# Performance work log

Hardware: AMD Instinct MI355X
Metric: run time of the kernel (lower is better)

The kernel has to match this reference:

```python
import jax, jax.numpy as jnp
import numpy as np

D = 2048      # d_model
H = 16        # kv_heads
G = 4         # num_groups
HPG = H // G  # heads per group
HD = D // H   # head dim = 128
B, S = 2, 2048


def setup_inputs() -> dict:
    key = jax.random.key(0)
    ks = jax.random.split(key, 5)
    def w(k, shape, fan_in):
        return jax.random.normal(k, shape, jnp.float32) * (fan_in ** -0.5)
    return {
        "x": jax.random.normal(ks[0], (B, S, D), jnp.float32),
        "attn_mask": jnp.ones((S, S), jnp.float32),
        "Wqkv": w(ks[1], (D, 3 * D), D),
        "bqkv": jnp.zeros((3 * D,), jnp.float32),
        "Wq": w(ks[2], (G, HD, HD), HD),   # shared per-group query proj
        "bq": jnp.zeros((G, HD), jnp.float32),
        "Wv": w(ks[3], (G, HD, HD), HD),   # shared per-group value proj
        "bv": jnp.zeros((G, HD), jnp.float32),
    }


def reference(x, attn_mask, Wqkv, bqkv, Wq, bq, Wv, bv):
    Bx, Sx, Dm = x.shape
    qkv = x @ Wqkv + bqkv                      # [B,S,3D]
    q, k, v = jnp.split(qkv, 3, axis=-1)       # each [B,S,D]
    q = q.reshape(Bx, Sx, G, HPG, HD)
    k = k.reshape(Bx, Sx, G, HPG, HD)
    v = v.reshape(Bx, Sx, G, HPG, HD)
    # shared per-group linear applied to every head slice in the group
    q = jnp.einsum('bsghd,gde->bsghe', q, Wq) + bq[None, None, :, None, :]
    v = jnp.einsum('bsghd,gde->bsghe', v, Wv) + bv[None, None, :, None, :]
    scale = HD ** -0.5
    scores = jnp.einsum('bqghd,bkghd->bghqk', q, k) * scale   # [B,G,HPG,S,S]
    attn = jax.nn.softmax(scores, axis=-1)
    attn = attn * attn_mask                    # post-softmax multiplicative mask
    out = jnp.einsum('bghqk,bkghd->bqghd', attn, v)            # [B,S,G,HPG,HD]
    return out.reshape(Bx, Sx, Dm)
```

## Files before the change

### kernel.cpp

```cpp
#include <hip/hip_runtime.h>

typedef __attribute__((ext_vector_type(8))) short short8;
typedef __attribute__((ext_vector_type(4))) float f32x4;
typedef __attribute__((ext_vector_type(4))) unsigned short ushort4v;
typedef unsigned long long u64;

#define DM 2048
#define ND 6144
#define SEQ 2048
#define HD 128
#define QSCALE (0.08838834764831845f * 1.4426950408889634f)

#define MFMA(a, b, c) __builtin_amdgcn_mfma_f32_16x16x32_bf16((a), (b), (c), 0, 0, 0)

__device__ __forceinline__ unsigned short f2bf(float f) {
  unsigned int u = __float_as_uint(f);
  return (unsigned short)((u + 0x7FFFu + ((u >> 16) & 1u)) >> 16);
}
__device__ __forceinline__ float bf2f(unsigned short h) {
  return __uint_as_float(((unsigned int)h) << 16);
}

__global__ void cvt_bf16_kernel(const float* __restrict__ src,
                                unsigned short* __restrict__ dst, int n4) {
  int i = blockIdx.x * blockDim.x + threadIdx.x;
  int st = gridDim.x * blockDim.x;
  for (; i < n4; i += st) {
    f32x4 v = ((const f32x4*)src)[i];
    ushort4v o;
    o[0] = f2bf(v[0]); o[1] = f2bf(v[1]); o[2] = f2bf(v[2]); o[3] = f2bf(v[3]);
    ((ushort4v*)dst)[i] = o;
  }
}

__global__ void transk_kernel(const float* __restrict__ Wqkv,
                              unsigned short* __restrict__ WbT) {
  __shared__ float tile[64 * 68];
  int bx = blockIdx.x;
  int dt = bx >> 5, ct = bx & 31;
  int d0 = dt * 64, c0 = ct * 64;
  int t = threadIdx.x;
#pragma unroll
  for (int j = 0; j < 4; ++j) {
    int el = (t + j * 256) * 4;
    int r = el >> 6, cc = el & 63;
    f32x4 v = *(const f32x4*)(Wqkv + (size_t)(d0 + r) * ND + 2048 + c0 + cc);
    *(f32x4*)(&tile[r * 68 + cc]) = v;
  }
  __syncthreads();
#pragma unroll
  for (int j = 0; j < 4; ++j) {
    int el = (t + j * 256) * 4;
    int c = el >> 6, dd = el & 63;
    ushort4v o;
#pragma unroll
    for (int i = 0; i < 4; ++i) o[i] = f2bf(tile[(dd + i) * 68 + c]);
    *(ushort4v*)(&WbT[(size_t)(2048 + c0 + c) * DM + d0 + dd]) = o;
  }
}

__global__ __launch_bounds__(256) void fold_kernel(const float* __restrict__ Wqkv,
                                                   const float* __restrict__ Wq,
                                                   const float* __restrict__ Wv,
                                                   unsigned short* __restrict__ WbT) {
  __shared__ float wm[128 * 64];
  __shared__ float wt[64 * 128];
  int bx = blockIdx.x;
  int p = bx >> 10;
  int head = (bx >> 6) & 15;
  int dt = (bx >> 1) & 31;
  int eh = bx & 1;
  int g = head >> 2;
  const float* Wm = (p ? Wv : Wq) + g * 16384;
  int cbase = p * 4096 + head * 128;
  int d0 = dt * 64;
  int t = threadIdx.x;
#pragma unroll
  for (int j = 0; j < 8; ++j) {
    int el = (t + j * 256) * 4;
    int dd = el >> 6, e = el & 63;
    *(f32x4*)(&wm[dd * 64 + e]) = *(const f32x4*)(Wm + dd * 128 + eh * 64 + e);
  }
#pragma unroll
  for (int j = 0; j < 8; ++j) {
    int el = (t + j * 256) * 4;
    int r = el >> 7, cc = el & 127;
    *(f32x4*)(&wt[r * 128 + cc]) =
        *(const f32x4*)(Wqkv + (size_t)(d0 + r) * ND + cbase + cc);
  }
  __syncthreads();
  int td = t >> 4, te = t & 15;
  int dl = td * 4, e0 = te * 4;
  float acc[4][4];
#pragma unroll
  for (int i = 0; i < 4; ++i)
#pragma unroll
    for (int j = 0; j < 4; ++j) acc[i][j] = 0.f;
  for (int dd = 0; dd < 128; ++dd) {
    f32x4 bv = *(const f32x4*)(&wm[dd * 64 + e0]);
#pragma unroll
    for (int i = 0; i < 4; ++i) {
      float a = wt[(dl + i) * 128 + dd];
#pragma unroll
      for (int j = 0; j < 4; ++j) acc[i][j] += a * bv[j];
    }
  }
  float sc = p ? 1.0f : QSCALE;
  int outcol0 = p * 4096 + head * 128 + eh * 64 + e0;
#pragma unroll
  for (int j = 0; j < 4; ++j) {
    ushort4v o;
#pragma unroll
    for (int i = 0; i < 4; ++i) o[i] = f2bf(acc[i][j] * sc);
    *(ushort4v*)(&WbT[(size_t)(outcol0 + j) * DM + d0 + dl]) = o;
  }
}

__global__ void bias_kernel(const float* __restrict__ bqkv, const float* __restrict__ Wq,
                            const float* __restrict__ bq, const float* __restrict__ Wv,
                            const float* __restrict__ bv, float* __restrict__ biasf) {
  int col = blockIdx.x * 256 + threadIdx.x;
  if (col >= ND) return;
  float v;
  if (col < 2048) {
    int g = col >> 9, e = col & 127, base = col & ~127;
    float s = 0.f;
    for (int dd = 0; dd < 128; ++dd) s += bqkv[base + dd] * Wq[g * 16384 + dd * 128 + e];
    v = (s + bq[g * 128 + e]) * QSCALE;
  } else if (col < 4096) {
    v = bqkv[col];
  } else {
    int cv = col - 4096;
    int g = cv >> 9, e = cv & 127, base = col & ~127;
    float s = 0.f;
    for (int dd = 0; dd < 128; ++dd) s += bqkv[base + dd] * Wv[g * 16384 + dd * 128 + e];
    v = s + bv[g * 128 + e];
  }
  biasf[col] = v;
}

__global__ __launch_bounds__(256) void gemm_kernel(
    const unsigned short* __restrict__ A, const unsigned short* __restrict__ Bt,
    const float* __restrict__ biasf, unsigned short* __restrict__ Qb,
    unsigned short* __restrict__ Kb, unsigned short* __restrict__ Vt) {
  __shared__ unsigned short As[128 * 32];
  __shared__ unsigned short Bs[128 * 32];
  int bid = blockIdx.x;
  int swz = (bid & 7) * 192 + (bid >> 3);
  int bm = swz & 31, bn = swz >> 5;
  int m0 = bm * 128, n0 = bn * 128;
  int tid = threadIdx.x, w = tid >> 6, l = tid & 63;
  int ln = l & 15, hi = l >> 4;
  int wr = w >> 1, wc = w & 1;

  int ob0 = w * 2048 + l * 16;
  int ob1 = ob0 + 1024;
  const unsigned short* a0 = A + (size_t)(m0 + (ob0 >> 6)) * DM + ((ob0 & 63) >> 1);
  const unsigned short* a1 = A + (size_t)(m0 + (ob1 >> 6)) * DM + ((ob1 & 63) >> 1);
  const unsigned short* b0 = Bt + (size_t)(n0 + (ob0 >> 6)) * DM + ((ob0 & 63) >> 1);
  const unsigned short* b1 = Bt + (size_t)(n0 + (ob1 >> 6)) * DM + ((ob1 & 63) >> 1);
  char* asb = (char*)(&As[0]);
  char* bsb = (char*)(&Bs[0]);

  f32x4 acc[4][4] = {};
  for (int kt = 0; kt < DM; kt += 32) {
    __syncthreads();
    __builtin_amdgcn_global_load_lds((const __attribute__((address_space(1))) void*)(a0 + kt),
                                     (__attribute__((address_space(3))) void*)(asb + w * 2048), 16, 0, 0);
    __builtin_amdgcn_global_load_lds((const __attribute__((address_space(1))) void*)(a1 + kt),
                                     (__attribute__((address_space(3))) void*)(asb + w * 2048 + 1024), 16, 0, 0);
    __builtin_amdgcn_global_load_lds((const __attribute__((address_space(1))) void*)(b0 + kt),
                                     (__attribute__((address_space(3))) void*)(bsb + w * 2048), 16, 0, 0);
    __builtin_amdgcn_global_load_lds((const __attribute__((address_space(1))) void*)(b1 + kt),
                                     (__attribute__((address_space(3))) void*)(bsb + w * 2048 + 1024), 16, 0, 0);
    __syncthreads();
    short8 af[4], bfm[4];
#pragma unroll
    for (int mi = 0; mi < 4; ++mi)
      af[mi] = *(const short8*)(&As[(wr * 64 + mi * 16 + ln) * 32 + hi * 8]);
#pragma unroll
    for (int ni = 0; ni < 4; ++ni)
      bfm[ni] = *(const short8*)(&Bs[(wc * 64 + ni * 16 + ln) * 32 + hi * 8]);
#pragma unroll
    for (int mi = 0; mi < 4; ++mi)
#pragma unroll
      for (int ni = 0; ni < 4; ++ni)
        acc[mi][ni] = MFMA(af[mi], bfm[ni], acc[mi][ni]);
  }

  int part = bn >> 4, head = bn & 15;
  int hbuf = (m0 >> 11) * 16 + head;
  int srow0 = (m0 & 2047) + wr * 64;
#pragma unroll
  for (int ni = 0; ni < 4; ++ni) {
    int col = wc * 64 + ni * 16 + ln;
    float bsv = biasf[n0 + col];
#pragma unroll
    for (int mi = 0; mi < 4; ++mi) {
      int srow = srow0 + mi * 16 + hi * 4;
      f32x4 v = acc[mi][ni];
      if (part == 2) {
        ushort4v o = {f2bf(v[0] + bsv), f2bf(v[1] + bsv), f2bf(v[2] + bsv), f2bf(v[3] + bsv)};
        *(ushort4v*)(&Vt[(size_t)(hbuf * 128 + col) * SEQ + srow]) = o;
      } else {
        unsigned short* dst = (part ? Kb : Qb) + ((size_t)hbuf * SEQ + srow) * HD + col;
        dst[0] = f2bf(v[0] + bsv);
        dst[HD] = f2bf(v[1] + bsv);
        dst[2 * HD] = f2bf(v[2] + bsv);
        dst[3 * HD] = f2bf(v[3] + bsv);
      }
    }
  }
}

__global__ __launch_bounds__(256, 2) void attn_kernel(
    const unsigned short* __restrict__ Qb, const unsigned short* __restrict__ Kb,
    const unsigned short* __restrict__ Vt, const unsigned short* __restrict__ Mb,
    float* __restrict__ out) {
  __shared__ unsigned short Ks[64 * 128];
  __shared__ unsigned short Vs[128 * 64];
  __shared__ unsigned short Ms[128 * 64];
  __shared__ unsigned short Ps[4][32 * 64];
  int bx = blockIdx.x;
  int hb = bx >> 4;
  int q0 = (bx & 15) * 128;
  int b = hb >> 4, head = hb & 15;
  int tid = threadIdx.x, w = tid >> 6, l = tid & 63;
  int ln = l & 15, hi = l >> 4;
  const unsigned short* Qh = Qb + ((size_t)hb * SEQ + q0 + w * 32) * HD;
  const unsigned short* Kh = Kb + (size_t)hb * SEQ * HD;
  const unsigned short* Vh = Vt + (size_t)hb * HD * SEQ;
  char* KsB = (char*)(&Ks[0]);
  char* VsB = (char*)(&Vs[0]);
  char* MsB = (char*)(&Ms[0]);
  char* PwB = (char*)(&Ps[w][0]);

  short8 qf[2][4];
#pragma unroll
  for (int qb = 0; qb < 2; ++qb)
#pragma unroll
    for (int kk = 0; kk < 4; ++kk)
      qf[qb][kk] = *(const short8*)(Qh + (qb * 16 + ln) * HD + kk * 32 + hi * 8);

  f32x4 acc[8][2] = {};
  float mrun[2] = {-1e30f, -1e30f}, Zrun[2] = {0.f, 0.f};

  for (int t = 0; t < 32; ++t) {
    int k0 = t * 64;
    __syncthreads();
    {
      int row = tid >> 2, seg = (tid & 3) * 64;
      const unsigned short* src = Kh + (size_t)(k0 + row) * HD + (seg >> 1);
      short8 tv[4];
#pragma unroll
      for (int j = 0; j < 4; ++j) tv[j] = *(const short8*)(src + j * 8);
#pragma unroll
      for (int j = 0; j < 4; ++j)
        *(short8*)(KsB + ((row * 256 + seg + j * 16) ^ ((row & 7) << 4))) = tv[j];
    }
    {
      int row = tid >> 1, seg = (tid & 1) * 64;
      const unsigned short* src = Vh + (size_t)row * SEQ + k0 + (seg >> 1);
      short8 tv[4];
#pragma unroll
      for (int j = 0; j < 4; ++j) tv[j] = *(const short8*)(src + j * 8);
#pragma unroll
      for (int j = 0; j < 4; ++j)
        *(short8*)(VsB + ((row * 128 + seg + j * 16) ^ ((row & 7) << 4))) = tv[j];
    }
    {
      int row = tid >> 1, seg = (tid & 1) * 64;
      const unsigned short* src = Mb + (size_t)(q0 + row) * SEQ + k0 + (seg >> 1);
      short8 tv[4];
#pragma unroll
      for (int j = 0; j < 4; ++j) tv[j] = *(const short8*)(src + j * 8);
#pragma unroll
      for (int j = 0; j < 4; ++j)
        *(short8*)(MsB + ((row * 128 + seg + j * 16) ^ ((row & 7) << 4))) = tv[j];
    }
    __syncthreads();

    f32x4 sAcc[4][2] = {};
#pragma unroll
    for (int kk = 0; kk < 4; ++kk) {
#pragma unroll
      for (int mb = 0; mb < 4; ++mb) {
        int key = mb * 16 + ln;
        short8 kf = *(const short8*)(KsB + ((key * 256 + kk * 64 + hi * 16) ^ ((key & 7) << 4)));
        sAcc[mb][0] = MFMA(kf, qf[0][kk], sAcc[mb][0]);
        sAcc[mb][1] = MFMA(kf, qf[1][kk], sAcc[mb][1]);
      }
    }

#pragma unroll
    for (int qb = 0; qb < 2; ++qb) {
      float tm = -1e30f;
#pragma unroll
      for (int mb = 0; mb < 4; ++mb)
#pragma unroll
        for (int r = 0; r < 4; ++r) tm = fmaxf(tm, sAcc[mb][qb][r]);
      tm = fmaxf(tm, __shfl_xor(tm, 16));
      tm = fmaxf(tm, __shfl_xor(tm, 32));
      float mn = fmaxf(mrun[qb], tm);
      float al = __builtin_amdgcn_exp2f(mrun[qb] - mn);
      mrun[qb] = mn;
      float ts = 0.f;
      int qrow = w * 32 + qb * 16 + ln;
      int swzm = (qrow & 7) << 4;
      int swzp = (ln & 7) << 4;
#pragma unroll
      for (int mb = 0; mb < 4; ++mb) {
        u64 mk = *(const u64*)(MsB + ((qrow * 128 + mb * 32 + hi * 8) ^ swzm));
        u64 pk = 0;
#pragma unroll
        for (int r = 0; r < 4; ++r) {
          float p = __builtin_amdgcn_exp2f(sAcc[mb][qb][r] - mn);
          ts += p;
          float pm = p * bf2f((unsigned short)(mk >> (16 * r)));
          pk |= ((u64)f2bf(pm)) << (16 * r);
        }
        *(u64*)(PwB + (((qb * 16 + ln) * 128 + mb * 32 + hi * 8) ^ swzp)) = pk;
      }
      ts += __shfl_xor(ts, 16);
      ts += __shfl_xor(ts, 32);
      Zrun[qb] = Zrun[qb] * al + ts;
#pragma unroll
      for (int db = 0; db < 8; ++db) acc[db][qb] *= al;
    }

#pragma unroll
    for (int kv = 0; kv < 2; ++kv) {
      short8 pf[2];
#pragma unroll
      for (int qb = 0; qb < 2; ++qb)
        pf[qb] = *(const short8*)(PwB + (((qb * 16 + ln) * 128 + kv * 64 + hi * 16) ^ ((ln & 7) << 4)));
#pragma unroll
      for (int db = 0; db < 8; ++db) {
        int d = db * 16 + ln;
        short8 vf = *(const short8*)(VsB + ((d * 128 + kv * 64 + hi * 16) ^ ((d & 7) << 4)));
        acc[db][0] = MFMA(vf, pf[0], acc[db][0]);
        acc[db][1] = MFMA(vf, pf[1], acc[db][1]);
      }
    }
  }

#pragma unroll
  for (int qb = 0; qb < 2; ++qb) {
    float rz = 1.0f / Zrun[qb];
    int srow = q0 + w * 32 + qb * 16 + ln;
    float* dst = out + ((size_t)(b * SEQ + srow)) * DM + head * HD + hi * 4;
#pragma unroll
    for (int db = 0; db < 8; ++db) {
      f32x4 o;
#pragma unroll
      for (int r = 0; r < 4; ++r) o[r] = acc[db][qb][r] * rz;
      *(f32x4*)(dst + db * 16) = o;
    }
  }
}

extern "C" void kernel_launch(void* const* d_in, const int* in_sizes, int n_in,
                              void* d_out, int out_size, void* d_ws, size_t ws_size,
                              hipStream_t stream) {
  (void)in_sizes; (void)n_in; (void)out_size; (void)ws_size;
  const float* x    = (const float*)d_in[0];
  const float* mask = (const float*)d_in[1];
  const float* Wqkv = (const float*)d_in[2];
  const float* bqkv = (const float*)d_in[3];
  const float* Wq   = (const float*)d_in[4];
  const float* bq   = (const float*)d_in[5];
  const float* Wv   = (const float*)d_in[6];
  const float* bv   = (const float*)d_in[7];
  float* out = (float*)d_out;
  char* ws = (char*)d_ws;

  unsigned short* xb    = (unsigned short*)(ws);
  unsigned short* maskb = (unsigned short*)(ws + 16777216);
  unsigned short* WbT   = (unsigned short*)(ws + 25165824);
  float*          biasf = (float*)(ws + 50331648);
  unsigned short* Qb    = (unsigned short*)(ws + 50356224);
  unsigned short* Kb    = (unsigned short*)(ws + 67133440);
  unsigned short* Vt    = (unsigned short*)(ws + 83910656);

  cvt_bf16_kernel<<<2048, 256, 0, stream>>>(x, xb, 2097152);
  cvt_bf16_kernel<<<1024, 256, 0, stream>>>(mask, maskb, 1048576);
  transk_kernel<<<1024, 256, 0, stream>>>(Wqkv, WbT);
  fold_kernel<<<2048, 256, 0, stream>>>(Wqkv, Wq, Wv, WbT);
  bias_kernel<<<24, 256, 0, stream>>>(bqkv, Wq, bq, Wv, bv, biasf);
  gemm_kernel<<<1536, 256, 0, stream>>>(xb, WbT, biasf, Qb, Kb, Vt);
  attn_kernel<<<512, 256, 0, stream>>>(Qb, Kb, Vt, maskb, out);
}
```

Baseline: 449.9 us.

## Rewrite QKV GEMM with 256x128 tiles, double-buffered swizzled LDS and prefetch

The QKV projection GEMM now uses 512-thread blocks on 256x128 output tiles with a K-step of 64. Operands are staged into two LDS buffers through global_load_lds, and the next tiles are prefetched while MFMAs run on the current one. An XOR swizzle on the LDS layout avoids bank conflicts, and s_setprio raises priority around the MFMA bursts. This targets load latency and the barrier stalls of the old single-buffer loop, at the cost of 96KB of dynamic LDS per block and hand-placed waitcnt/barrier ordering that could be fragile.

New measurement: 430.9 us. 1.04x faster.

```diff
diff --git a/kernel.cpp b/kernel.cpp
--- a/kernel.cpp
+++ b/kernel.cpp
@@ -139,71 +139,108 @@
   biasf[col] = v;
 }
 
-__global__ __launch_bounds__(256) void gemm_kernel(
+__global__ __launch_bounds__(512, 2) void gemm_kernel(
     const unsigned short* __restrict__ A, const unsigned short* __restrict__ Bt,
     const float* __restrict__ biasf, unsigned short* __restrict__ Qb,
     unsigned short* __restrict__ Kb, unsigned short* __restrict__ Vt) {
-  __shared__ unsigned short As[128 * 32];
-  __shared__ unsigned short Bs[128 * 32];
+  extern __shared__ char lds[];
   int bid = blockIdx.x;
-  int swz = (bid & 7) * 192 + (bid >> 3);
-  int bm = swz & 31, bn = swz >> 5;
-  int m0 = bm * 128, n0 = bn * 128;
-  int tid = threadIdx.x, w = tid >> 6, l = tid & 63;
-  int ln = l & 15, hi = l >> 4;
-  int wr = w >> 1, wc = w & 1;
-
-  int ob0 = w * 2048 + l * 16;
-  int ob1 = ob0 + 1024;
-  const unsigned short* a0 = A + (size_t)(m0 + (ob0 >> 6)) * DM + ((ob0 & 63) >> 1);
-  const unsigned short* a1 = A + (size_t)(m0 + (ob1 >> 6)) * DM + ((ob1 & 63) >> 1);
-  const unsigned short* b0 = Bt + (size_t)(n0 + (ob0 >> 6)) * DM + ((ob0 & 63) >> 1);
-  const unsigned short* b1 = Bt + (size_t)(n0 + (ob1 >> 6)) * DM + ((ob1 & 63) >> 1);
-  char* asb = (char*)(&As[0]);
-  char* bsb = (char*)(&Bs[0]);
+  int swz = (bid & 7) * 96 + (bid >> 3);
+  int bm = swz & 15, bn = swz >> 4;
+  int m0 = bm * 256, n0 = bn * 128;
+  int tid = threadIdx.x;
+  int wid = tid >> 6, lane = tid & 63;
+  int ln = lane & 15, hi = lane >> 4;
+  int wr = wid >> 1, wc = wid & 1;
+
+  int soff[6];
+#pragma unroll
+  for (int j = 0; j < 6; ++j) {
+    int d = (j < 4 ? j * 8192 : (j - 4) * 8192) + tid * 16;
+    int row = d >> 7;
+    int p = d ^ ((row & 7) << 4);
+    int kof = (p & 127) >> 1;
+    soff[j] = (j < 4 ? (m0 + row) : (n0 + row)) * DM + kof;
+  }
+  auto stage = [&](int buf, int kel) {
+#pragma unroll
+    for (int j = 0; j < 6; ++j) {
+      const unsigned short* s = (j < 4 ? A : Bt) + soff[j] + kel;
+      char* dlds = lds + buf * 49152 +
+                   (j < 4 ? j * 8192 : 32768 + (j - 4) * 8192) + wid * 1024;
+      __builtin_amdgcn_global_load_lds(
+          (const __attribute__((address_space(1))) void*)s,
+          (__attribute__((address_space(3))) void*)dlds, 16, 0, 0);
+    }
+  };
 
   f32x4 acc[4][4] = {};
-  for (int kt = 0; kt < DM; kt += 32) {
-    __syncthreads();
-    __builtin_amdgcn_global_load_lds((const __attribute__((address_space(1))) void*)(a0 + kt),
-                                     (__attribute__((address_space(3))) void*)(asb + w * 2048), 16, 0, 0);
-    __builtin_amdgcn_global_load_lds((const __attribute__((address_space(1))) void*)(a1 + kt),
-                                     (__attribute__((address_space(3))) void*)(asb + w * 2048 + 1024), 16, 0, 0);
-    __builtin_amdgcn_global_load_lds((const __attribute__((address_space(1))) void*)(b0 + kt),
-                                     (__attribute__((address_space(3))) void*)(bsb + w * 2048), 16, 0, 0);
-    __builtin_amdgcn_global_load_lds((const __attribute__((address_space(1))) void*)(b1 + kt),
-                                     (__attribute__((address_space(3))) void*)(bsb + w * 2048 + 1024), 16, 0, 0);
-    __syncthreads();
-    short8 af[4], bfm[4];
+  const int swzl = (ln & 7) << 4;
+  int arow0 = wr * 64 + ln;
+  int brow0 = wc * 64 + ln;
+
+  stage(0, 0);
+  stage(1, 64);
+  asm volatile("s_waitcnt vmcnt(6)" ::: "memory");
+  asm volatile("s_barrier" ::: "memory");
+
+  for (int t = 0; t < 32; ++t) {
+    char* base = lds + (t & 1) * 49152;
+    short8 a0[4], b0[4], a1[4], b1[4];
 #pragma unroll
     for (int mi = 0; mi < 4; ++mi)
-      af[mi] = *(const short8*)(&As[(wr * 64 + mi * 16 + ln) * 32 + hi * 8]);
+      a0[mi] = *(const short8*)(base + (((arow0 + mi * 16) * 128 + hi * 16) ^ swzl));
 #pragma unroll
     for (int ni = 0; ni < 4; ++ni)
-      bfm[ni] = *(const short8*)(&Bs[(wc * 64 + ni * 16 + ln) * 32 + hi * 8]);
+      b0[ni] = *(const short8*)(base + 32768 + (((brow0 + ni * 16) * 128 + hi * 16) ^ swzl));
+    __builtin_amdgcn_s_setprio(1);
 #pragma unroll
     for (int mi = 0; mi < 4; ++mi)
 #pragma unroll
       for (int ni = 0; ni < 4; ++ni)
-        acc[mi][ni] = MFMA(af[mi], bfm[ni], acc[mi][ni]);
-  }
-
-  int part = bn >> 4, head = bn & 15;
-  int hbuf = (m0 >> 11) * 16 + head;
-  int srow0 = (m0 & 2047) + wr * 64;
+        acc[mi][ni] = MFMA(a0[mi], b0[ni], acc[mi][ni]);
+    __builtin_amdgcn_s_setprio(0);
+#pragma unroll
+    for (int mi = 0; mi < 4; ++mi)
+      a1[mi] = *(const short8*)(base + (((arow0 + mi * 16) * 128 + 64 + hi * 16) ^ swzl));
+#pragma unroll
+    for (int ni = 0; ni < 4; ++ni)
+      b1[ni] = *(const short8*)(base + 32768 + (((brow0 + ni * 16) * 128 + 64 + hi * 16) ^ swzl));
+    asm volatile("s_waitcnt lgkmcnt(0)" ::: "memory");
+    asm volatile("s_barrier" ::: "memory");
+    if (t < 30) stage(t & 1, (t + 2) * 64);
+    __builtin_amdgcn_s_setprio(1);
+#pragma unroll
+    for (int mi = 0; mi < 4; ++mi)
+#pragma unroll
+      for (int ni = 0; ni < 4; ++ni)
+        acc[mi][ni] = MFMA(a1[mi], b1[ni], acc[mi][ni]);
+    __builtin_amdgcn_s_setprio(0);
+    if (t < 30) {
+      asm volatile("s_waitcnt vmcnt(6)" ::: "memory");
+    } else if (t == 30) {
+      asm volatile("s_waitcnt vmcnt(0)" ::: "memory");
+    }
+    if (t < 31) asm volatile("s_barrier" ::: "memory");
+  }
+
+  int part = n0 >> 11;
+  int head = (n0 >> 7) & 15;
+  int batch = m0 >> 11;
+  int hbuf = batch * 16 + head;
 #pragma unroll
   for (int ni = 0; ni < 4; ++ni) {
-    int col = wc * 64 + ni * 16 + ln;
-    float bsv = biasf[n0 + col];
+    int dcol = wc * 64 + ni * 16 + ln;
+    float bsv = biasf[n0 + dcol];
 #pragma unroll
     for (int mi = 0; mi < 4; ++mi) {
-      int srow = srow0 + mi * 16 + hi * 4;
+      int srow = (m0 & 2047) + wr * 64 + mi * 16 + hi * 4;
       f32x4 v = acc[mi][ni];
       if (part == 2) {
         ushort4v o = {f2bf(v[0] + bsv), f2bf(v[1] + bsv), f2bf(v[2] + bsv), f2bf(v[3] + bsv)};
-        *(ushort4v*)(&Vt[(size_t)(hbuf * 128 + col) * SEQ + srow]) = o;
+        *(ushort4v*)(&Vt[(size_t)(hbuf * 128 + dcol) * SEQ + srow]) = o;
       } else {
-        unsigned short* dst = (part ? Kb : Qb) + ((size_t)hbuf * SEQ + srow) * HD + col;
+        unsigned short* dst = (part ? Kb : Qb) + ((size_t)hbuf * SEQ + srow) * HD + dcol;
         dst[0] = f2bf(v[0] + bsv);
         dst[HD] = f2bf(v[1] + bsv);
         dst[2 * HD] = f2bf(v[2] + bsv);
@@ -382,11 +419,14 @@
   unsigned short* Kb    = (unsigned short*)(ws + 67133440);
   unsigned short* Vt    = (unsigned short*)(ws + 83910656);
 
+  hipFuncSetAttribute((const void*)gemm_kernel,
+                      hipFuncAttributeMaxDynamicSharedMemorySize, 98304);
+
   cvt_bf16_kernel<<<2048, 256, 0, stream>>>(x, xb, 2097152);
   cvt_bf16_kernel<<<1024, 256, 0, stream>>>(mask, maskb, 1048576);
   transk_kernel<<<1024, 256, 0, stream>>>(Wqkv, WbT);
   fold_kernel<<<2048, 256, 0, stream>>>(Wqkv, Wq, Wv, WbT);
   bias_kernel<<<24, 256, 0, stream>>>(bqkv, Wq, bq, Wv, bv, biasf);
-  gemm_kernel<<<1536, 256, 0, stream>>>(xb, WbT, biasf, Qb, Kb, Vt);
+  gemm_kernel<<<768, 512, 98304, stream>>>(xb, WbT, biasf, Qb, Kb, Vt);
   attn_kernel<<<512, 256, 0, stream>>>(Qb, Kb, Vt, maskb, out);
 }
```
